# Kernel tuning notes

Measured on AMD Instinct MI355X. Metric: run time of the kernel, lower is better.

The kernel has to match this reference:

```python
import jax, jax.numpy as jnp
import numpy as np

N_NODES = 100000
N_EDGES = 1600000
HIDDEN = 128


def setup_inputs() -> dict:
    key = jax.random.key(0)
    ks = jax.random.split(key, 10)
    inp = {
        "hidden_states": jax.random.normal(ks[0], (N_NODES, HIDDEN), dtype=jnp.float32),
        "edges_i": jax.random.randint(ks[1], (2, N_EDGES), 0, N_NODES, dtype=jnp.int64),
        "edges_ii": jax.random.randint(ks[2], (2, N_EDGES), 0, N_NODES, dtype=jnp.int64),
        "edges_iii": jax.random.randint(ks[3], (2, N_EDGES), 0, N_NODES, dtype=jnp.int64),
        "edges_a": jax.random.randint(ks[4], (2, N_EDGES), 0, N_NODES, dtype=jnp.int64),
        # GCNConv weights (hidden -> hidden), no bias, Glorot-like init
        "W_i": jax.random.normal(ks[5], (HIDDEN, HIDDEN), dtype=jnp.float32) / np.sqrt(HIDDEN),
        "W_ii": jax.random.normal(ks[6], (HIDDEN, HIDDEN), dtype=jnp.float32) / np.sqrt(HIDDEN),
        "W_iii": jax.random.normal(ks[7], (HIDDEN, HIDDEN), dtype=jnp.float32) / np.sqrt(HIDDEN),
        "W_a": jax.random.normal(ks[8], (HIDDEN, HIDDEN), dtype=jnp.float32) / np.sqrt(HIDDEN),
    }
    return inp


def _gcn_conv(x, W, edges):
    # GCNConv with normalize=False, add_self_loops=False, bias=False:
    # out[dst] = sum over edges (x @ W)[src]
    xw = x @ W                                   # [N, H] small GEMM
    msg = jnp.take(xw, edges[0], axis=0)         # gather at src: [E, H]
    return jax.ops.segment_sum(msg, edges[1], num_segments=x.shape[0])


def reference(hidden_states, edges_i, edges_ii, edges_iii, edges_a, W_i, W_ii, W_iii, W_a):
    # VariationalNormalEpanechnikovDropout acts as identity in eval mode.
    x = hidden_states
    out = _gcn_conv(x, W_i, edges_i)
    out = out + _gcn_conv(x, W_ii, edges_ii)
    out = out + _gcn_conv(x, W_iii, edges_iii)
    out = out + _gcn_conv(x, W_a, edges_a)
    return out
```

## Files before the change

### kernel.cpp

```cpp
#include <hip/hip_runtime.h>


#define H 128

typedef __bf16 bf16x8 __attribute__((ext_vector_type(8)));
typedef float f32x4 __attribute__((ext_vector_type(4)));

static __device__ __forceinline__ ushort f2bf(float f) {
  union { float f; uint u; } v; v.f = f;
  uint r = (v.u + 0x7FFFu + ((v.u >> 16) & 1u)) >> 16;
  return (ushort)r;
}
static __device__ __forceinline__ float bflo(uint u) {
  union { uint u; float f; } v; v.u = u << 16; return v.f;
}
static __device__ __forceinline__ float bfhi(uint u) {
  union { uint u; float f; } v; v.u = u & 0xFFFF0000u; return v.f;
}

__global__ __launch_bounds__(256) void prep_w(const float* __restrict__ W0,
                                              const float* __restrict__ W1,
                                              const float* __restrict__ W2,
                                              const float* __restrict__ W3,
                                              ushort* __restrict__ Wt) {
  int idx = blockIdx.x * 256 + threadIdx.x;
  int kk = idx & 127;
  int c = (idx >> 7) & 127;
  int k = idx >> 14;
  const float* W = (k == 0) ? W0 : (k == 1) ? W1 : (k == 2) ? W2 : W3;
  Wt[idx] = f2bf(W[kk * 128 + c]);
}

__global__ __launch_bounds__(256) void conv_x(const float4* __restrict__ X4,
                                              uint2* __restrict__ Xb2, int m) {
  int i = blockIdx.x * 256 + threadIdx.x;
  if (i < m) {
    float4 v = X4[i];
    uint2 p;
    p.x = (uint)f2bf(v.x) | ((uint)f2bf(v.y) << 16);
    p.y = (uint)f2bf(v.z) | ((uint)f2bf(v.w) << 16);
    Xb2[i] = p;
  }
}

static __device__ __forceinline__ void fetch_edge(
    int gid, int c1, int c2, int c3,
    const int* d0, const int* d1, const int* d2, const int* d3,
    const int* s0, const int* s1, const int* s2, const int* s3,
    int& dst, int& src, int& k) {
  int i;
  const int *dp, *sp;
  if (gid < c1)      { k = 0; i = gid;      dp = d0; sp = s0; }
  else if (gid < c2) { k = 1; i = gid - c1; dp = d1; sp = s1; }
  else if (gid < c3) { k = 2; i = gid - c2; dp = d2; sp = s2; }
  else               { k = 3; i = gid - c3; dp = d3; sp = s3; }
  dst = dp[i];
  src = sp[i];
}

#define EPB 4096

__global__ __launch_bounds__(256) void part_count(
    const int* __restrict__ d0, const int* __restrict__ d1,
    const int* __restrict__ d2, const int* __restrict__ d3,
    int c1, int c2, int c3, int tot, int nbin, int* __restrict__ hb) {
  __shared__ int lh[512];
  for (int i = threadIdx.x; i < nbin; i += 256) lh[i] = 0;
  __syncthreads();
  int base = blockIdx.x * EPB;
#pragma unroll
  for (int u = 0; u < 16; ++u) {
    int gid = base + u * 256 + threadIdx.x;
    if (gid < tot) {
      int i;
      const int* dp;
      if (gid < c1)      { i = gid;      dp = d0; }
      else if (gid < c2) { i = gid - c1; dp = d1; }
      else if (gid < c3) { i = gid - c2; dp = d2; }
      else               { i = gid - c3; dp = d3; }
      atomicAdd(&lh[dp[i] >> 8], 1);
    }
  }
  __syncthreads();
  int* row = hb + (size_t)blockIdx.x * nbin;
  for (int i = threadIdx.x; i < nbin; i += 256) row[i] = lh[i];
}

__global__ __launch_bounds__(256) void part_scanA(int* __restrict__ hb,
                                                  int nblk, int nbin,
                                                  int* __restrict__ btot) {
  __shared__ int ws4[4];
  const int bin = blockIdx.x;
  const int t = threadIdx.x, lane = t & 63, wid = t >> 6;
  const int C = (nblk + 255) / 256;
  int b0 = t * C;
  int b1 = min(b0 + C, nblk);
  int s = 0;
  for (int b = b0; b < b1; ++b) s += hb[(size_t)b * nbin + bin];
  int incl = s;
#pragma unroll
  for (int d = 1; d < 64; d <<= 1) {
    int x = __shfl_up(incl, d, 64);
    if (lane >= d) incl += x;
  }
  if (lane == 63) ws4[wid] = incl;
  __syncthreads();
  if (t == 0) {
    int run = 0;
#pragma unroll
    for (int i = 0; i < 4; ++i) { int v = ws4[i]; ws4[i] = run; run += v; }
  }
  __syncthreads();
  int run = ws4[wid] + (incl - s);
  for (int b = b0; b < b1; ++b) {
    int v = hb[(size_t)b * nbin + bin];
    hb[(size_t)b * nbin + bin] = run;
    run += v;
  }
  if (t == 255) btot[bin] = run;
}

__global__ __launch_bounds__(512) void part_scanB(const int* __restrict__ btot,
                                                  int* __restrict__ binbase,
                                                  int nbin) {
  __shared__ int ws8[8];
  const int t = threadIdx.x, lane = t & 63, wid = t >> 6;
  int v = (t < nbin) ? btot[t] : 0;
  int incl = v;
#pragma unroll
  for (int d = 1; d < 64; d <<= 1) {
    int x = __shfl_up(incl, d, 64);
    if (lane >= d) incl += x;
  }
  if (lane == 63) ws8[wid] = incl;
  __syncthreads();
  if (t == 0) {
    int run = 0;
#pragma unroll
    for (int i = 0; i < 8; ++i) { int v2 = ws8[i]; ws8[i] = run; run += v2; }
  }
  __syncthreads();
  int excl = ws8[wid] + (incl - v);
  if (t < nbin) binbase[t] = excl;
  if (t == nbin - 1) binbase[nbin] = excl + v;
}

__global__ __launch_bounds__(256) void part_scatter(
    const int* __restrict__ d0, const int* __restrict__ d1,
    const int* __restrict__ d2, const int* __restrict__ d3,
    const int* __restrict__ s0, const int* __restrict__ s1,
    const int* __restrict__ s2, const int* __restrict__ s3,
    int c1, int c2, int c3, int tot, int nbin,
    const int* __restrict__ hb, const int* __restrict__ binbase,
    uint* __restrict__ part) {
  __shared__ int cur[512];
  const int* row = hb + (size_t)blockIdx.x * nbin;
  for (int i = threadIdx.x; i < nbin; i += 256) cur[i] = binbase[i] + row[i];
  __syncthreads();
  int base = blockIdx.x * EPB;
#pragma unroll
  for (int u = 0; u < 16; ++u) {
    int gid = base + u * 256 + threadIdx.x;
    if (gid < tot) {
      int dst, src, k;
      fetch_edge(gid, c1, c2, c3, d0, d1, d2, d3, s0, s1, s2, s3, dst, src, k);
      int pos = atomicAdd(&cur[dst >> 8], 1);
      part[pos] = (uint)src | ((uint)(((dst & 255) << 2) | k) << 17);
    }
  }
}

__global__ __launch_bounds__(1024) void build_bucket(
    const uint* __restrict__ part, const int* __restrict__ binbase,
    int n4, int* __restrict__ rp4, int* __restrict__ col_idx) {
  __shared__ int lh[1024];
  __shared__ int ws16[16];
  const int b = blockIdx.x;
  const int beg = binbase[b], end = binbase[b + 1];
  const int t = threadIdx.x, lane = t & 63, wid = t >> 6;

  lh[t] = 0;
  __syncthreads();
  for (int i = beg + t; i < end; i += 1024)
    atomicAdd(&lh[part[i] >> 17], 1);
  __syncthreads();

  int v = lh[t];
  int incl = v;
#pragma unroll
  for (int d = 1; d < 64; d <<= 1) {
    int x = __shfl_up(incl, d, 64);
    if (lane >= d) incl += x;
  }
  if (lane == 63) ws16[wid] = incl;
  __syncthreads();
  if (t == 0) {
    int run = 0;
#pragma unroll
    for (int i = 0; i < 16; ++i) { int w = ws16[i]; ws16[i] = run; run += w; }
  }
  __syncthreads();
  int excl = ws16[wid] + (incl - v);
  lh[t] = beg + excl;

  int gseg = b * 1024 + t;
  if (gseg <= n4) rp4[gseg] = beg + excl;
  __syncthreads();

  for (int i = beg + t; i < end; i += 1024) {
    uint e = part[i];
    int pos = atomicAdd(&lh[e >> 17], 1);
    col_idx[pos] = (int)(e & 0x1FFFFu);
  }
}

__global__ __launch_bounds__(256, 8) void gg(const uint* __restrict__ Xb,
                                             const int* __restrict__ rp4,
                                             const int* __restrict__ col_idx,
                                             const ushort* __restrict__ Wt,
                                             float* __restrict__ out, int n) {
  __shared__ uint sS[16][258];

  const int node0 = blockIdx.x * 16;
  const int wave = threadIdx.x >> 6;
  const int lane = threadIdx.x & 63;

#pragma unroll
  for (int i = 0; i < 4; ++i) {
    int local = wave * 4 + i;
    int node = node0 + local;
    if (node < n) {
      const int* rp = rp4 + (size_t)node * 4;
#pragma unroll
      for (int k = 0; k < 4; ++k) {
        int beg = rp[k], end = rp[k + 1];
        float ax = 0.f, ay = 0.f, bx = 0.f, by = 0.f;
        float cx = 0.f, cy = 0.f, dx = 0.f, dy = 0.f;
        int j = beg;
        for (; j + 7 < end; j += 8) {
          int e0 = col_idx[j], e1 = col_idx[j + 1];
          int e2 = col_idx[j + 2], e3 = col_idx[j + 3];
          int e4 = col_idx[j + 4], e5 = col_idx[j + 5];
          int e6 = col_idx[j + 6], e7 = col_idx[j + 7];
          uint u0 = Xb[(size_t)e0 * 64 + lane];
          uint u1 = Xb[(size_t)e1 * 64 + lane];
          uint u2 = Xb[(size_t)e2 * 64 + lane];
          uint u3 = Xb[(size_t)e3 * 64 + lane];
          uint u4 = Xb[(size_t)e4 * 64 + lane];
          uint u5 = Xb[(size_t)e5 * 64 + lane];
          uint u6 = Xb[(size_t)e6 * 64 + lane];
          uint u7 = Xb[(size_t)e7 * 64 + lane];
          ax += bflo(u0); ay += bfhi(u0);
          bx += bflo(u1); by += bfhi(u1);
          cx += bflo(u2); cy += bfhi(u2);
          dx += bflo(u3); dy += bfhi(u3);
          ax += bflo(u4); ay += bfhi(u4);
          bx += bflo(u5); by += bfhi(u5);
          cx += bflo(u6); cy += bfhi(u6);
          dx += bflo(u7); dy += bfhi(u7);
        }
        for (; j + 1 < end; j += 2) {
          int e0 = col_idx[j], e1 = col_idx[j + 1];
          uint u0 = Xb[(size_t)e0 * 64 + lane];
          uint u1 = Xb[(size_t)e1 * 64 + lane];
          ax += bflo(u0); ay += bfhi(u0);
          bx += bflo(u1); by += bfhi(u1);
        }
        if (j < end) {
          uint u = Xb[(size_t)col_idx[j] * 64 + lane];
          ax += bflo(u); ay += bfhi(u);
        }
        float rx = (ax + bx) + (cx + dx);
        float ry = (ay + by) + (cy + dy);
        sS[local][k * 64 + lane] = (uint)f2bf(rx) | ((uint)f2bf(ry) << 16);
      }
    } else {
#pragma unroll
      for (int k = 0; k < 4; ++k) sS[local][k * 64 + lane] = 0u;
    }
  }
  __syncthreads();

  const ushort* sSu = (const ushort*)&sS[0][0];
  const int lr = lane & 15;
  const int lg = lane >> 4;
  const int cf0 = wave * 2;

  f32x4 acc0 = (f32x4)0.f, acc1 = (f32x4)0.f;

#pragma unroll
  for (int kc = 0; kc < 4; ++kc) {
#pragma unroll
    for (int k4 = 0; k4 < 4; ++k4) {
      bf16x8 a = *(const bf16x8*)&sSu[lr * 516 + kc * 128 + k4 * 32 + lg * 8];
      bf16x8 b0 = *(const bf16x8*)&Wt[kc * 16384 + (cf0 * 16 + lr) * 128 + k4 * 32 + lg * 8];
      bf16x8 b1 = *(const bf16x8*)&Wt[kc * 16384 + ((cf0 + 1) * 16 + lr) * 128 + k4 * 32 + lg * 8];
      acc0 = __builtin_amdgcn_mfma_f32_16x16x32_bf16(a, b0, acc0, 0, 0, 0);
      acc1 = __builtin_amdgcn_mfma_f32_16x16x32_bf16(a, b1, acc1, 0, 0, 0);
    }
  }

#pragma unroll
  for (int r = 0; r < 4; ++r) {
    int row = node0 + lg * 4 + r;
    if (row < n) {
      out[(size_t)row * H + cf0 * 16 + lr] = acc0[r];
      out[(size_t)row * H + (cf0 + 1) * 16 + lr] = acc1[r];
    }
  }
}

extern "C" void kernel_launch(void* const* d_in, const int* in_sizes, int n_in,
                              void* d_out, int out_size, void* d_ws, size_t ws_size,
                              hipStream_t stream) {
  const float* X = (const float*)d_in[0];
  const int* edges[4] = {(const int*)d_in[1], (const int*)d_in[2],
                         (const int*)d_in[3], (const int*)d_in[4]};
  const float* Wk[4] = {(const float*)d_in[5], (const float*)d_in[6],
                        (const float*)d_in[7], (const float*)d_in[8]};
  float* out = (float*)d_out;

  int n = in_sizes[0] / H;
  int nE[4];
  int tot = 0;
  for (int k = 0; k < 4; ++k) {
    nE[k] = in_sizes[1 + k] / 2;
    tot += nE[k];
  }
  int c1 = nE[0], c2 = c1 + nE[1], c3 = c2 + nE[2];
  int n4 = n * 4;
  int nbin = (n + 255) / 256;
  int nblk = (tot + EPB - 1) / EPB;

  char* ws = (char*)d_ws;
  size_t off = 0;
  auto take = [&](size_t bytes) -> char* {
    char* p = ws + off;
    off = (off + bytes + 255) & ~(size_t)255;
    return p;
  };
  ushort* Wt = (ushort*)take(4 * 128 * 128 * sizeof(ushort));
  uint* Xb = (uint*)take((size_t)n * H * sizeof(ushort));
  int* hb = (int*)take((size_t)nblk * nbin * sizeof(int));
  int* btot = (int*)take((size_t)nbin * sizeof(int));
  int* binbase = (int*)take((size_t)(nbin + 1) * sizeof(int));
  int* rp4 = (int*)take((size_t)(n4 + 1) * sizeof(int));
  uint* part = (uint*)take((size_t)tot * sizeof(uint));
  int* col_idx = (int*)take((size_t)tot * sizeof(int));

  const int* s0 = edges[0];
  const int* d0 = edges[0] + nE[0];
  const int* s1 = edges[1];
  const int* d1 = edges[1] + nE[1];
  const int* s2 = edges[2];
  const int* d2 = edges[2] + nE[2];
  const int* s3 = edges[3];
  const int* d3 = edges[3] + nE[3];

  prep_w<<<256, 256, 0, stream>>>(Wk[0], Wk[1], Wk[2], Wk[3], Wt);
  conv_x<<<(n * 32 + 255) / 256, 256, 0, stream>>>((const float4*)X, (uint2*)Xb, n * 32);

  part_count<<<nblk, 256, 0, stream>>>(d0, d1, d2, d3, c1, c2, c3, tot, nbin, hb);
  part_scanA<<<nbin, 256, 0, stream>>>(hb, nblk, nbin, btot);
  part_scanB<<<1, 512, 0, stream>>>(btot, binbase, nbin);
  part_scatter<<<nblk, 256, 0, stream>>>(d0, d1, d2, d3, s0, s1, s2, s3,
                                         c1, c2, c3, tot, nbin, hb, binbase, part);
  build_bucket<<<nbin, 1024, 0, stream>>>(part, binbase, n4, rp4, col_idx);

  gg<<<(n + 15) / 16, 256, 0, stream>>>(Xb, rp4, col_idx, Wt, out, n);
}
```

Baseline: 467.8 us.

## Gather rows with 16-byte loads over four edges per wave and shuffle-broadcast indices

The aggregation loop now splits each wave into four 16-lane groups, and each group loads a full 256-byte bf16 row using uint4 loads, so four edges are fetched per instruction instead of one edge per instruction at 4 bytes per lane. Edge indices are prefetched with one coalesced load per segment and broadcast with shuffles, replacing the scalar col_idx loads. The partial sums are combined with cross-group xor shuffles before being written to shared memory. This adds shuffle and reduction overhead per segment and leaves lanes idle on short tails, and the outer loop is no longer unrolled.

```diff
diff --git a/kernel.cpp b/kernel.cpp
--- a/kernel.cpp
+++ b/kernel.cpp
@@ -214,6 +214,14 @@
   }
 }
 
+#define ACC8(u)                                                       \
+  do {                                                                \
+    a0 += bflo((u).x); a1 += bfhi((u).x);                             \
+    a2 += bflo((u).y); a3 += bfhi((u).y);                             \
+    a4 += bflo((u).z); a5 += bfhi((u).z);                             \
+    a6 += bflo((u).w); a7 += bfhi((u).w);                             \
+  } while (0)
+
 __global__ __launch_bounds__(256, 8) void gg(const uint* __restrict__ Xb,
                                              const int* __restrict__ rp4,
                                              const int* __restrict__ col_idx,
@@ -224,55 +232,71 @@
   const int node0 = blockIdx.x * 16;
   const int wave = threadIdx.x >> 6;
   const int lane = threadIdx.x & 63;
-
-#pragma unroll
+  const int g = lane >> 4;
+  const int qb = (lane & 15) * 4;
+
+#pragma unroll 1
   for (int i = 0; i < 4; ++i) {
     int local = wave * 4 + i;
     int node = node0 + local;
     if (node < n) {
-      const int* rp = rp4 + (size_t)node * 4;
+      const int4 rpv = *(const int4*)(rp4 + (size_t)node * 4);
+      const int rpE = rp4[(size_t)node * 4 + 4];
+      int pe0 = (rpv.x + lane < rpv.y) ? col_idx[rpv.x + lane] : 0;
+      int pe1 = (rpv.y + lane < rpv.z) ? col_idx[rpv.y + lane] : 0;
+      int pe2 = (rpv.z + lane < rpv.w) ? col_idx[rpv.z + lane] : 0;
+      int pe3 = (rpv.w + lane < rpE)   ? col_idx[rpv.w + lane] : 0;
 #pragma unroll
       for (int k = 0; k < 4; ++k) {
-        int beg = rp[k], end = rp[k + 1];
-        float ax = 0.f, ay = 0.f, bx = 0.f, by = 0.f;
-        float cx = 0.f, cy = 0.f, dx = 0.f, dy = 0.f;
-        int j = beg;
-        for (; j + 7 < end; j += 8) {
-          int e0 = col_idx[j], e1 = col_idx[j + 1];
-          int e2 = col_idx[j + 2], e3 = col_idx[j + 3];
-          int e4 = col_idx[j + 4], e5 = col_idx[j + 5];
-          int e6 = col_idx[j + 6], e7 = col_idx[j + 7];
-          uint u0 = Xb[(size_t)e0 * 64 + lane];
-          uint u1 = Xb[(size_t)e1 * 64 + lane];
-          uint u2 = Xb[(size_t)e2 * 64 + lane];
-          uint u3 = Xb[(size_t)e3 * 64 + lane];
-          uint u4 = Xb[(size_t)e4 * 64 + lane];
-          uint u5 = Xb[(size_t)e5 * 64 + lane];
-          uint u6 = Xb[(size_t)e6 * 64 + lane];
-          uint u7 = Xb[(size_t)e7 * 64 + lane];
-          ax += bflo(u0); ay += bfhi(u0);
-          bx += bflo(u1); by += bfhi(u1);
-          cx += bflo(u2); cy += bfhi(u2);
-          dx += bflo(u3); dy += bfhi(u3);
-          ax += bflo(u4); ay += bfhi(u4);
-          bx += bflo(u5); by += bfhi(u5);
-          cx += bflo(u6); cy += bfhi(u6);
-          dx += bflo(u7); dy += bfhi(u7);
+        int beg = (k == 0) ? rpv.x : (k == 1) ? rpv.y : (k == 2) ? rpv.z : rpv.w;
+        int end = (k == 0) ? rpv.y : (k == 1) ? rpv.z : (k == 2) ? rpv.w : rpE;
+        int pe  = (k == 0) ? pe0   : (k == 1) ? pe1   : (k == 2) ? pe2   : pe3;
+        int len = end - beg;
+        int m = (len > 64) ? 64 : len;
+        float a0 = 0.f, a1 = 0.f, a2 = 0.f, a3 = 0.f;
+        float a4 = 0.f, a5 = 0.f, a6 = 0.f, a7 = 0.f;
+        int s = 0;
+        for (; s + 8 <= m; s += 8) {
+          int ea = __shfl(pe, s + g, 64);
+          int eb = __shfl(pe, s + 4 + g, 64);
+          uint4 ua = *(const uint4*)&Xb[(size_t)ea * 64 + qb];
+          uint4 ub = *(const uint4*)&Xb[(size_t)eb * 64 + qb];
+          ACC8(ua);
+          ACC8(ub);
         }
-        for (; j + 1 < end; j += 2) {
-          int e0 = col_idx[j], e1 = col_idx[j + 1];
-          uint u0 = Xb[(size_t)e0 * 64 + lane];
-          uint u1 = Xb[(size_t)e1 * 64 + lane];
-          ax += bflo(u0); ay += bfhi(u0);
-          bx += bflo(u1); by += bfhi(u1);
+        for (; s < m; s += 4) {
+          int li = s + g;
+          int e = __shfl(pe, li, 64);
+          if (li < m) {
+            uint4 u = *(const uint4*)&Xb[(size_t)e * 64 + qb];
+            ACC8(u);
+          }
         }
-        if (j < end) {
-          uint u = Xb[(size_t)col_idx[j] * 64 + lane];
-          ax += bflo(u); ay += bfhi(u);
+        if (len > 64) {
+          for (int j = beg + 64; j < end; j += 4) {
+            int li = j + g;
+            if (li < end) {
+              int e = col_idx[li];
+              uint4 u = *(const uint4*)&Xb[(size_t)e * 64 + qb];
+              ACC8(u);
+            }
+          }
         }
-        float rx = (ax + bx) + (cx + dx);
-        float ry = (ay + by) + (cy + dy);
-        sS[local][k * 64 + lane] = (uint)f2bf(rx) | ((uint)f2bf(ry) << 16);
+        a0 += __shfl_xor(a0, 16, 64); a0 += __shfl_xor(a0, 32, 64);
+        a1 += __shfl_xor(a1, 16, 64); a1 += __shfl_xor(a1, 32, 64);
+        a2 += __shfl_xor(a2, 16, 64); a2 += __shfl_xor(a2, 32, 64);
+        a3 += __shfl_xor(a3, 16, 64); a3 += __shfl_xor(a3, 32, 64);
+        a4 += __shfl_xor(a4, 16, 64); a4 += __shfl_xor(a4, 32, 64);
+        a5 += __shfl_xor(a5, 16, 64); a5 += __shfl_xor(a5, 32, 64);
+        a6 += __shfl_xor(a6, 16, 64); a6 += __shfl_xor(a6, 32, 64);
+        a7 += __shfl_xor(a7, 16, 64); a7 += __shfl_xor(a7, 32, 64);
+        if (lane < 16) {
+          uint* drow = &sS[local][k * 64 + qb];
+          drow[0] = (uint)f2bf(a0) | ((uint)f2bf(a1) << 16);
+          drow[1] = (uint)f2bf(a2) | ((uint)f2bf(a3) << 16);
+          drow[2] = (uint)f2bf(a4) | ((uint)f2bf(a5) << 16);
+          drow[3] = (uint)f2bf(a6) | ((uint)f2bf(a7) << 16);
+        }
       }
     } else {
 #pragma unroll
```

After: 416.6 us. 10.9% less time.
